# Kernel optimization log

Hardware: AMD Instinct MI355X
Metric: run time of the kernel (lower is better)

Reference implementation:

```python
import jax, jax.numpy as jnp
import numpy as np

WS = 7        # window size (square)
SH = 3        # shift size
NH = 8        # num heads
N = WS * WS   # tokens per window


def _rel_pos_index():
    coords = np.stack(np.meshgrid(np.arange(WS), np.arange(WS), indexing='ij'))
    cf = coords.reshape(2, -1)                      # (2, N)
    rel = cf[:, :, None] - cf[:, None, :]           # (2, N, N)
    rel = rel.transpose(1, 2, 0)
    rel[:, :, 0] += WS - 1
    rel[:, :, 1] += WS - 1
    rel[:, :, 0] *= 2 * WS - 1
    return rel.sum(-1)                              # (N, N) int


def _attn_mask(pH, pW):
    img = np.zeros((pH, pW), dtype=np.float32)
    h_sl = [(0, pH - WS), (pH - WS, pH - SH), (pH - SH, pH)]
    w_sl = [(0, pW - WS), (pW - WS, pW - SH), (pW - SH, pW)]
    cnt = 0
    for h0, h1 in h_sl:
        for w0, w1 in w_sl:
            img[h0:h1, w0:w1] = cnt
            cnt += 1
    m = img.reshape(pH // WS, WS, pW // WS, WS).transpose(0, 2, 1, 3).reshape(-1, N)
    diff = m[:, None, :] - m[:, :, None]            # (nw, N, N)
    return np.where(diff != 0, -100.0, 0.0).astype(np.float32)


def setup_inputs() -> dict:
    key = jax.random.key(0)
    ks = jax.random.split(key, 6)
    C = 256
    return {
        'x': jax.random.normal(ks[0], (32, 56, 56, C), dtype=jnp.float32),
        'qkv_weight': jax.random.normal(ks[1], (3 * C, C), dtype=jnp.float32) * 0.02,
        'qkv_bias': jax.random.normal(ks[2], (3 * C,), dtype=jnp.float32) * 0.02,
        'proj_weight': jax.random.normal(ks[3], (C, C), dtype=jnp.float32) * 0.02,
        'proj_bias': jax.random.normal(ks[4], (C,), dtype=jnp.float32) * 0.02,
        'rpb_table': jax.random.normal(ks[5], ((2 * WS - 1) ** 2, NH), dtype=jnp.float32) * 0.02,
    }


def reference(x, qkv_weight, qkv_bias, proj_weight, proj_bias, rpb_table):
    B, H, W, C = x.shape
    hd = C // NH
    pad_r = (WS - W % WS) % WS
    pad_b = (WS - H % WS) % WS
    xp = jnp.pad(x, ((0, 0), (0, pad_b), (0, pad_r), (0, 0)))
    pH, pW = H + pad_b, W + pad_r
    xp = jnp.roll(xp, shift=(-SH, -SH), axis=(1, 2))
    nw = (pH // WS) * (pW // WS)
    # window partition -> (B*nw, N, C)
    xw = xp.reshape(B, pH // WS, WS, pW // WS, WS, C)
    xw = xw.transpose(0, 1, 3, 2, 4, 5).reshape(B * nw, N, C)
    # qkv projection
    qkv = xw @ qkv_weight.T + qkv_bias                      # (B*nw, N, 3C)
    qkv = qkv.reshape(B * nw, N, 3, NH, hd).transpose(2, 0, 3, 1, 4)
    q, k, v = qkv[0], qkv[1], qkv[2]                        # (B*nw, NH, N, hd)
    q = q * (hd ** -0.5)
    attn = jnp.einsum('bhnd,bhmd->bhnm', q, k)              # (B*nw, NH, N, N)
    # relative position bias
    idx = jnp.asarray(_rel_pos_index())
    bias = rpb_table[idx].transpose(2, 0, 1)                # (NH, N, N)
    attn = attn + bias[None]
    # shift mask
    mask = jnp.asarray(_attn_mask(pH, pW))                  # (nw, N, N)
    attn = attn.reshape(B, nw, NH, N, N) + mask[None, :, None]
    attn = jax.nn.softmax(attn.reshape(B * nw, NH, N, N), axis=-1)
    out = jnp.einsum('bhnm,bhmd->bhnd', attn, v)            # (B*nw, NH, N, hd)
    out = out.transpose(0, 2, 1, 3).reshape(B * nw, N, C)
    out = out @ proj_weight.T + proj_bias
    # window reverse
    out = out.reshape(B, pH // WS, pW // WS, WS, WS, C)
    out = out.transpose(0, 1, 3, 2, 4, 5).reshape(B, pH, pW, C)
    out = jnp.roll(out, shift=(SH, SH), axis=(1, 2))
    return out[:, :H, :W, :]
```

## Files before the change

### kernel.cpp

```cpp
#include <hip/hip_runtime.h>
#include <hip/hip_bf16.h>

typedef __attribute__((ext_vector_type(4))) float f32x4;
typedef __attribute__((ext_vector_type(8))) short s16x8;
typedef __attribute__((ext_vector_type(4))) short s16x4;

#define LQS 520
#define FOS 260
#define VTS 72
#define LAS 264

#define OFF_A    0
#define SZ_A     (64 * LQS * 2)
#define OFF_B    (OFF_A + SZ_A)
#define SZ_B     (256 * VTS * 2)
#define OFF_BIAS (OFF_B + SZ_B)
#define SZ_BIAS  6096
#define OFF_ML   (OFF_BIAS + SZ_BIAS)
#define SZ_ML    (8 * 2 * 64 * 2 * 4)
#define SMEM_BYTES (OFF_ML + SZ_ML)

__device__ __forceinline__ short f2bf(float f) {
    unsigned u = __builtin_bit_cast(unsigned, f);
    unsigned r = (u + 0x7FFFu + ((u >> 16) & 1u)) >> 16;
    return (short)r;
}

__device__ __forceinline__ unsigned pk2bf(float a, float b) {
    return (unsigned)(unsigned short)f2bf(a) | ((unsigned)(unsigned short)f2bf(b) << 16);
}

__device__ __forceinline__ int region_id(int wy, int wx, int ty, int tx) {
    int rr = wy * 7 + ty;
    int cc = wx * 7 + tx;
    int rh = (rr < 49) ? 0 : ((rr < 53) ? 1 : 2);
    int rw = (cc < 49) ? 0 : ((cc < 53) ? 1 : 2);
    return rh * 3 + rw;
}

__global__ void wcvt_kernel(const float* __restrict__ qw, const float* __restrict__ pw,
                            short* __restrict__ wqkv, short* __restrict__ wproj) {
    int idx = blockIdx.x * blockDim.x + threadIdx.x;
    int stride = gridDim.x * blockDim.x;
    for (int i = idx; i < 65536; i += stride) {
        if (i < 49152) {
            const f32x4 v = *(const f32x4*)(qw + i * 4);
            s16x4 o = { f2bf(v.x), f2bf(v.y), f2bf(v.z), f2bf(v.w) };
            *(s16x4*)(wqkv + i * 4) = o;
        } else {
            int j = i - 49152;
            const f32x4 v = *(const f32x4*)(pw + j * 4);
            s16x4 o = { f2bf(v.x), f2bf(v.y), f2bf(v.z), f2bf(v.w) };
            *(s16x4*)(wproj + j * 4) = o;
        }
    }
}

__global__ __launch_bounds__(1024, 4)
void swin_kernel(const float* __restrict__ x,
                 const float* __restrict__ qkv_bias,
                 const float* __restrict__ proj_bias,
                 const float* __restrict__ rpb,
                 const short* __restrict__ wqkv,
                 const short* __restrict__ wproj,
                 float* __restrict__ out) {
    __shared__ __align__(16) char smem[SMEM_BYTES];
    short* lqk   = (short*)(smem + OFF_A);
    float* lout  = (float*)(smem + OFF_A);
    short* lvt   = (short*)(smem + OFF_B);
    short* la    = (short*)(smem + OFF_B);
    float* lbias = (float*)(smem + OFF_BIAS);
    float* lml   = (float*)(smem + OFF_ML);

    const int tid  = threadIdx.x;
    const int w    = tid >> 6;
    const int lane = tid & 63;
    const int il   = lane & 15;
    const int gl   = lane >> 4;
    const int hh   = w >> 1;
    const int jh   = w & 1;

    const int b   = blockIdx.x >> 6;
    const int wid = blockIdx.x & 63;
    const int wy  = wid >> 3, wx = wid & 7;

    for (int i = tid; i < 1352; i += 1024) lbias[(i >> 3) * 9 + (i & 7)] = rpb[i];
    for (int i = tid; i < 4096; i += 1024) {
        int t = i >> 6, c4 = (i & 63) << 2;
        s16x4 o;
        if (t < 49) {
            int ty = t / 7, tx = t % 7;
            int R = wy * 7 + ty + 3; if (R >= 56) R -= 56;
            int C = wx * 7 + tx + 3; if (C >= 56) C -= 56;
            const f32x4 v = *(const f32x4*)(x + (((b * 56 + R) * 56 + C) << 8) + c4);
            o = (s16x4){ f2bf(v.x), f2bf(v.y), f2bf(v.z), f2bf(v.w) };
        } else {
            o = (s16x4){ 0, 0, 0, 0 };
        }
        *(s16x4*)&lqk[t * LQS + c4] = o;
    }
    __syncthreads();

    {
        f32x4 acc[4][3];
        #pragma unroll
        for (int mi = 0; mi < 4; mi++)
            #pragma unroll
            for (int t = 0; t < 3; t++) acc[mi][t] = (f32x4){0.f, 0.f, 0.f, 0.f};
        for (int k0 = 0; k0 < 256; k0 += 32) {
            s16x8 a[4];
            #pragma unroll
            for (int mi = 0; mi < 4; mi++)
                a[mi] = *(const s16x8*)&lqk[(mi * 16 + il) * LQS + k0 + 8 * gl];
            #pragma unroll
            for (int t = 0; t < 3; t++) {
                s16x8 bfr = *(const s16x8*)(wqkv + (t * 256 + 16 * w + il) * 256 + k0 + 8 * gl);
                #pragma unroll
                for (int mi = 0; mi < 4; mi++)
                    acc[mi][t] = __builtin_amdgcn_mfma_f32_16x16x32_bf16(a[mi], bfr, acc[mi][t], 0, 0, 0);
            }
        }
        {
            float bv = qkv_bias[512 + 16 * w + il];
            #pragma unroll
            for (int mi = 0; mi < 4; mi++) {
                s16x4 pk = { f2bf(acc[mi][2][0] + bv), f2bf(acc[mi][2][1] + bv),
                             f2bf(acc[mi][2][2] + bv), f2bf(acc[mi][2][3] + bv) };
                *(s16x4*)&lvt[(16 * w + il) * VTS + mi * 16 + gl * 4] = pk;
            }
        }
        __syncthreads();
        {
            float bq_ = qkv_bias[16 * w + il];
            float bk_ = qkv_bias[256 + 16 * w + il];
            #pragma unroll
            for (int mi = 0; mi < 4; mi++)
                #pragma unroll
                for (int r = 0; r < 4; r++) {
                    int row = mi * 16 + gl * 4 + r;
                    lqk[row * LQS + 16 * w + il] = f2bf((acc[mi][0][r] + bq_) * 0.17677669529663687f);
                    lqk[row * LQS + 256 + 16 * w + il] = f2bf(acc[mi][1][r] + bk_);
                }
        }
    }
    __syncthreads();

    f32x4 s[2][4];
    {
        s16x8 bq[4], ak[2];
        #pragma unroll
        for (int ni = 0; ni < 4; ni++)
            bq[ni] = *(const s16x8*)&lqk[(ni * 16 + il) * LQS + 32 * hh + 8 * gl];
        #pragma unroll
        for (int mi = 0; mi < 2; mi++)
            ak[mi] = *(const s16x8*)&lqk[(jh * 32 + mi * 16 + il) * LQS + 256 + 32 * hh + 8 * gl];
        #pragma unroll
        for (int mi = 0; mi < 2; mi++)
            #pragma unroll
            for (int ni = 0; ni < 4; ni++)
                s[mi][ni] = __builtin_amdgcn_mfma_f32_16x16x32_bf16(ak[mi], bq[ni], (f32x4){0.f,0.f,0.f,0.f}, 0, 0, 0);
    }
    int base9[4], cnti[4];
    #pragma unroll
    for (int ni = 0; ni < 4; ni++) {
        int i = ni * 16 + il; int ic = i > 48 ? 48 : i;
        int yi = ic / 7, xi = ic % 7;
        base9[ni] = (yi * 13 + xi + 84) * 9 + hh;
        cnti[ni] = region_id(wy, wx, yi, xi);
    }
    float mx[4] = { -1e30f, -1e30f, -1e30f, -1e30f };
    #pragma unroll
    for (int mi = 0; mi < 2; mi++) {
        #pragma unroll
        for (int r = 0; r < 4; r++) {
            int j = 32 * jh + mi * 16 + gl * 4 + r;
            bool jok = (j < 49);
            int jc = jok ? j : 48;
            int yj = jc / 7, xj = jc % 7;
            int bj9 = (yj * 13 + xj) * 9;
            int cj = region_id(wy, wx, yj, xj);
            #pragma unroll
            for (int ni = 0; ni < 4; ni++) {
                float v;
                if (jok) {
                    float bb = lbias[base9[ni] - bj9];
                    v = s[mi][ni][r] + bb + ((cnti[ni] != cj) ? -100.0f : 0.0f);
                } else {
                    v = -1e30f;
                }
                s[mi][ni][r] = v;
                mx[ni] = fmaxf(mx[ni], v);
            }
        }
    }
    #pragma unroll
    for (int ni = 0; ni < 4; ni++) {
        mx[ni] = fmaxf(mx[ni], __shfl_xor(mx[ni], 16));
        mx[ni] = fmaxf(mx[ni], __shfl_xor(mx[ni], 32));
    }
    float sm[4] = { 0.f, 0.f, 0.f, 0.f };
    #pragma unroll
    for (int mi = 0; mi < 2; mi++)
        #pragma unroll
        for (int ni = 0; ni < 4; ni++)
            #pragma unroll
            for (int r = 0; r < 4; r++) {
                float p = __expf(s[mi][ni][r] - mx[ni]);
                s[mi][ni][r] = p;
                sm[ni] += p;
            }
    #pragma unroll
    for (int ni = 0; ni < 4; ni++) {
        sm[ni] += __shfl_xor(sm[ni], 16);
        sm[ni] += __shfl_xor(sm[ni], 32);
    }
    if (gl == 0) {
        #pragma unroll
        for (int ni = 0; ni < 4; ni++) {
            int idx = ((hh * 2 + jh) * 64 + ni * 16 + il) * 2;
            lml[idx] = mx[ni];
            lml[idx + 1] = sm[ni];
        }
    }
    __syncthreads();
    float scale[4];
    #pragma unroll
    for (int ni = 0; ni < 4; ni++) {
        int idx = ((hh * 2 + (jh ^ 1)) * 64 + ni * 16 + il) * 2;
        float m_o = lml[idx], l_o = lml[idx + 1];
        float m_g = fmaxf(mx[ni], m_o);
        float l_g = sm[ni] * __expf(mx[ni] - m_g) + l_o * __expf(m_o - m_g);
        scale[ni] = __expf(mx[ni] - m_g) / l_g;
    }
    f32x4 o[2][4];
    {
        unsigned pkd[2][4][2];
        #pragma unroll
        for (int mi = 0; mi < 2; mi++)
            #pragma unroll
            for (int ni = 0; ni < 4; ni++) {
                pkd[mi][ni][0] = pk2bf(s[mi][ni][0] * scale[ni], s[mi][ni][1] * scale[ni]);
                pkd[mi][ni][1] = pk2bf(s[mi][ni][2] * scale[ni], s[mi][ni][3] * scale[ni]);
            }
        s16x8 av[2];
        #pragma unroll
        for (int md = 0; md < 2; md++)
            av[md] = *(const s16x8*)&lvt[(32 * hh + md * 16 + il) * VTS + jh * 32 + 8 * gl];
        #pragma unroll
        for (int ni = 0; ni < 4; ni++) {
            unsigned wd[4];
            #pragma unroll
            for (int q = 0; q < 4; q++) {
                int src = (2 * (gl & 1) + (q >> 1)) * 16 + il;
                unsigned v0 = (unsigned)__shfl((int)pkd[0][ni][q & 1], src);
                unsigned v1 = (unsigned)__shfl((int)pkd[1][ni][q & 1], src);
                wd[q] = (gl & 2) ? v1 : v0;
            }
            union { unsigned u[4]; s16x8 v; } cv;
            cv.u[0] = wd[0]; cv.u[1] = wd[1]; cv.u[2] = wd[2]; cv.u[3] = wd[3];
            #pragma unroll
            for (int md = 0; md < 2; md++)
                o[md][ni] = __builtin_amdgcn_mfma_f32_16x16x32_bf16(av[md], cv.v, (f32x4){0.f,0.f,0.f,0.f}, 0, 0, 0);
        }
    }
    if (jh == 0) {
        #pragma unroll
        for (int md = 0; md < 2; md++)
            #pragma unroll
            for (int ni = 0; ni < 4; ni++)
                *(f32x4*)&lout[(ni * 16 + il) * FOS + 32 * hh + md * 16 + gl * 4] = o[md][ni];
    }
    __syncthreads();
    if (jh == 1) {
        #pragma unroll
        for (int md = 0; md < 2; md++)
            #pragma unroll
            for (int ni = 0; ni < 4; ni++) {
                f32x4 t = *(const f32x4*)&lout[(ni * 16 + il) * FOS + 32 * hh + md * 16 + gl * 4];
                t.x += o[md][ni][0]; t.y += o[md][ni][1];
                t.z += o[md][ni][2]; t.w += o[md][ni][3];
                s16x4 pk = { f2bf(t.x), f2bf(t.y), f2bf(t.z), f2bf(t.w) };
                *(s16x4*)&la[(ni * 16 + il) * LAS + 32 * hh + md * 16 + gl * 4] = pk;
            }
    }
    __syncthreads();

    {
        f32x4 acc[4];
        #pragma unroll
        for (int mi = 0; mi < 4; mi++) acc[mi] = (f32x4){0.f, 0.f, 0.f, 0.f};
        for (int k0 = 0; k0 < 256; k0 += 32) {
            s16x8 bw = *(const s16x8*)(wproj + (16 * w + il) * 256 + k0 + 8 * gl);
            #pragma unroll
            for (int mi = 0; mi < 4; mi++) {
                s16x8 a = *(const s16x8*)&la[(mi * 16 + il) * LAS + k0 + 8 * gl];
                acc[mi] = __builtin_amdgcn_mfma_f32_16x16x32_bf16(a, bw, acc[mi], 0, 0, 0);
            }
        }
        float pb = proj_bias[16 * w + il];
        float* fout = lout;
        #pragma unroll
        for (int mi = 0; mi < 4; mi++)
            #pragma unroll
            for (int r = 0; r < 4; r++) {
                int t = mi * 16 + gl * 4 + r;
                if (t < 49) fout[t * FOS + 16 * w + il] = acc[mi][r] + pb;
            }
    }
    __syncthreads();
    for (int i = tid; i < 3136; i += 1024) {
        int t = i >> 6, c4 = (i & 63) << 2;
        f32x4 v = *(const f32x4*)&lout[t * FOS + c4];
        int ty = t / 7, tx = t % 7;
        int R = wy * 7 + ty + 3; if (R >= 56) R -= 56;
        int C = wx * 7 + tx + 3; if (C >= 56) C -= 56;
        *(f32x4*)(out + (((b * 56 + R) * 56 + C) << 8) + c4) = v;
    }
}

extern "C" void kernel_launch(void* const* d_in, const int* in_sizes, int n_in,
                              void* d_out, int out_size, void* d_ws, size_t ws_size,
                              hipStream_t stream) {
    const float* x   = (const float*)d_in[0];
    const float* qw  = (const float*)d_in[1];
    const float* qb  = (const float*)d_in[2];
    const float* pw  = (const float*)d_in[3];
    const float* pb  = (const float*)d_in[4];
    const float* rpb = (const float*)d_in[5];

    short* wqkv  = (short*)d_ws;
    short* wproj = wqkv + 768 * 256;

    wcvt_kernel<<<128, 256, 0, stream>>>(qw, pw, wqkv, wproj);
    swin_kernel<<<2048, 1024, 0, stream>>>(x, qb, pb, rpb, wqkv, wproj, (float*)d_out);
}
```

Measured before the change: 231.5 us.

## Precompute bias+mask table, fold into MFMA accumulator, drop softmax max pass

A new pre-kernel builds a combined relative-position-bias and shift-mask table for the four window classes, pre-scaled by log2(e). The attention kernel loads it as the MFMA accumulator init. It also folds log2(e) into the q scale, uses exp2 without subtracting the row max, and applies deferred normalization after PV. Float-to-bf16 conversion now uses the hardware packed convert instruction. These changes remove per-element index math, the max reduction and the cross-wave max exchange. Skipping the max subtraction risks overflow if scores are large.

```diff
diff --git a/kernel.cpp b/kernel.cpp
--- a/kernel.cpp
+++ b/kernel.cpp
@@ -14,28 +14,14 @@
 #define SZ_A     (64 * LQS * 2)
 #define OFF_B    (OFF_A + SZ_A)
 #define SZ_B     (256 * VTS * 2)
-#define OFF_BIAS (OFF_B + SZ_B)
-#define SZ_BIAS  6096
-#define OFF_ML   (OFF_BIAS + SZ_BIAS)
-#define SZ_ML    (8 * 2 * 64 * 2 * 4)
+#define OFF_ML   (OFF_B + SZ_B)
+#define SZ_ML    (8 * 64 * 4)
 #define SMEM_BYTES (OFF_ML + SZ_ML)
 
-__device__ __forceinline__ short f2bf(float f) {
-    unsigned u = __builtin_bit_cast(unsigned, f);
-    unsigned r = (u + 0x7FFFu + ((u >> 16) & 1u)) >> 16;
-    return (short)r;
-}
-
-__device__ __forceinline__ unsigned pk2bf(float a, float b) {
-    return (unsigned)(unsigned short)f2bf(a) | ((unsigned)(unsigned short)f2bf(b) << 16);
-}
-
-__device__ __forceinline__ int region_id(int wy, int wx, int ty, int tx) {
-    int rr = wy * 7 + ty;
-    int cc = wx * 7 + tx;
-    int rh = (rr < 49) ? 0 : ((rr < 53) ? 1 : 2);
-    int rw = (cc < 49) ? 0 : ((cc < 53) ? 1 : 2);
-    return rh * 3 + rw;
+__device__ __forceinline__ unsigned cvt2bf(float a, float b) {
+    unsigned r;
+    asm("v_cvt_pk_bf16_f32 %0, %1, %2" : "=v"(r) : "v"(a), "v"(b));
+    return r;
 }
 
 __global__ void wcvt_kernel(const float* __restrict__ qw, const float* __restrict__ pw,
@@ -43,33 +29,51 @@
     int idx = blockIdx.x * blockDim.x + threadIdx.x;
     int stride = gridDim.x * blockDim.x;
     for (int i = idx; i < 65536; i += stride) {
-        if (i < 49152) {
-            const f32x4 v = *(const f32x4*)(qw + i * 4);
-            s16x4 o = { f2bf(v.x), f2bf(v.y), f2bf(v.z), f2bf(v.w) };
-            *(s16x4*)(wqkv + i * 4) = o;
-        } else {
-            int j = i - 49152;
-            const f32x4 v = *(const f32x4*)(pw + j * 4);
-            s16x4 o = { f2bf(v.x), f2bf(v.y), f2bf(v.z), f2bf(v.w) };
-            *(s16x4*)(wproj + j * 4) = o;
-        }
-    }
+        const float* src = (i < 49152) ? (qw + i * 4) : (pw + (i - 49152) * 4);
+        unsigned* dst = (unsigned*)((i < 49152) ? (wqkv + i * 4) : (wproj + (i - 49152) * 4));
+        const f32x4 v = *(const f32x4*)src;
+        uint2 o = { cvt2bf(v.x, v.y), cvt2bf(v.z, v.w) };
+        *(uint2*)dst = o;
+    }
+}
+
+__global__ void bmgen_kernel(const float* __restrict__ rpb, float* __restrict__ bm) {
+    int idx = blockIdx.x * blockDim.x + threadIdx.x;
+    if (idx >= 131072) return;
+    int j = idx & 63;
+    int i = (idx >> 6) & 63;
+    int h = (idx >> 12) & 7;
+    int c = idx >> 15;
+    int cy = c >> 1, cx = c & 1;
+    float v;
+    if (j >= 49) {
+        v = -1e9f;
+    } else {
+        int ic = i > 48 ? 48 : i;
+        int yi = ic / 7, xi = ic % 7;
+        int yj = j / 7, xj = j % 7;
+        float bias = rpb[((yi - yj + 6) * 13 + (xi - xj + 6)) * 8 + h];
+        int ri = (cy ? (yi < 4 ? 1 : 2) : 0) * 3 + (cx ? (xi < 4 ? 1 : 2) : 0);
+        int rj = (cy ? (yj < 4 ? 1 : 2) : 0) * 3 + (cx ? (xj < 4 ? 1 : 2) : 0);
+        float mask = (ri != rj) ? -100.0f : 0.0f;
+        v = (bias + mask) * 1.4426950408889634f;
+    }
+    bm[idx] = v;
 }
 
 __global__ __launch_bounds__(1024, 4)
 void swin_kernel(const float* __restrict__ x,
                  const float* __restrict__ qkv_bias,
                  const float* __restrict__ proj_bias,
-                 const float* __restrict__ rpb,
                  const short* __restrict__ wqkv,
                  const short* __restrict__ wproj,
+                 const float* __restrict__ bm,
                  float* __restrict__ out) {
     __shared__ __align__(16) char smem[SMEM_BYTES];
     short* lqk   = (short*)(smem + OFF_A);
     float* lout  = (float*)(smem + OFF_A);
     short* lvt   = (short*)(smem + OFF_B);
     short* la    = (short*)(smem + OFF_B);
-    float* lbias = (float*)(smem + OFF_BIAS);
     float* lml   = (float*)(smem + OFF_ML);
 
     const int tid  = threadIdx.x;
@@ -84,20 +88,19 @@
     const int wid = blockIdx.x & 63;
     const int wy  = wid >> 3, wx = wid & 7;
 
-    for (int i = tid; i < 1352; i += 1024) lbias[(i >> 3) * 9 + (i & 7)] = rpb[i];
     for (int i = tid; i < 4096; i += 1024) {
         int t = i >> 6, c4 = (i & 63) << 2;
-        s16x4 o;
+        uint2 o;
         if (t < 49) {
             int ty = t / 7, tx = t % 7;
             int R = wy * 7 + ty + 3; if (R >= 56) R -= 56;
             int C = wx * 7 + tx + 3; if (C >= 56) C -= 56;
             const f32x4 v = *(const f32x4*)(x + (((b * 56 + R) * 56 + C) << 8) + c4);
-            o = (s16x4){ f2bf(v.x), f2bf(v.y), f2bf(v.z), f2bf(v.w) };
+            o.x = cvt2bf(v.x, v.y); o.y = cvt2bf(v.z, v.w);
         } else {
-            o = (s16x4){ 0, 0, 0, 0 };
-        }
-        *(s16x4*)&lqk[t * LQS + c4] = o;
+            o.x = 0; o.y = 0;
+        }
+        *(uint2*)&lqk[t * LQS + c4] = o;
     }
     __syncthreads();
 
@@ -124,25 +127,35 @@
             float bv = qkv_bias[512 + 16 * w + il];
             #pragma unroll
             for (int mi = 0; mi < 4; mi++) {
-                s16x4 pk = { f2bf(acc[mi][2][0] + bv), f2bf(acc[mi][2][1] + bv),
-                             f2bf(acc[mi][2][2] + bv), f2bf(acc[mi][2][3] + bv) };
-                *(s16x4*)&lvt[(16 * w + il) * VTS + mi * 16 + gl * 4] = pk;
+                uint2 pk = { cvt2bf(acc[mi][2][0] + bv, acc[mi][2][1] + bv),
+                             cvt2bf(acc[mi][2][2] + bv, acc[mi][2][3] + bv) };
+                *(uint2*)&lvt[(16 * w + il) * VTS + mi * 16 + gl * 4] = pk;
             }
         }
         __syncthreads();
         {
             float bq_ = qkv_bias[16 * w + il];
             float bk_ = qkv_bias[256 + 16 * w + il];
+            const float QSCL = 0.17677669529663687f * 1.4426950408889634f;
             #pragma unroll
             for (int mi = 0; mi < 4; mi++)
                 #pragma unroll
                 for (int r = 0; r < 4; r++) {
                     int row = mi * 16 + gl * 4 + r;
-                    lqk[row * LQS + 16 * w + il] = f2bf((acc[mi][0][r] + bq_) * 0.17677669529663687f);
-                    lqk[row * LQS + 256 + 16 * w + il] = f2bf(acc[mi][1][r] + bk_);
+                    unsigned u = cvt2bf((acc[mi][0][r] + bq_) * QSCL, acc[mi][1][r] + bk_);
+                    lqk[row * LQS + 16 * w + il] = (short)u;
+                    lqk[row * LQS + 256 + 16 * w + il] = (short)(u >> 16);
                 }
         }
     }
+    const int cls = ((wy == 7) ? 2 : 0) + ((wx == 7) ? 1 : 0);
+    const float* bmp = bm + ((cls * 8 + hh) * 64) * 64;
+    f32x4 ci[2][4];
+    #pragma unroll
+    for (int mi = 0; mi < 2; mi++)
+        #pragma unroll
+        for (int ni = 0; ni < 4; ni++)
+            ci[mi][ni] = *(const f32x4*)&bmp[(ni * 16 + il) * 64 + jh * 32 + mi * 16 + gl * 4];
     __syncthreads();
 
     f32x4 s[2][4];
@@ -158,45 +171,7 @@
         for (int mi = 0; mi < 2; mi++)
             #pragma unroll
             for (int ni = 0; ni < 4; ni++)
-                s[mi][ni] = __builtin_amdgcn_mfma_f32_16x16x32_bf16(ak[mi], bq[ni], (f32x4){0.f,0.f,0.f,0.f}, 0, 0, 0);
-    }
-    int base9[4], cnti[4];
-    #pragma unroll
-    for (int ni = 0; ni < 4; ni++) {
-        int i = ni * 16 + il; int ic = i > 48 ? 48 : i;
-        int yi = ic / 7, xi = ic % 7;
-        base9[ni] = (yi * 13 + xi + 84) * 9 + hh;
-        cnti[ni] = region_id(wy, wx, yi, xi);
-    }
-    float mx[4] = { -1e30f, -1e30f, -1e30f, -1e30f };
-    #pragma unroll
-    for (int mi = 0; mi < 2; mi++) {
-        #pragma unroll
-        for (int r = 0; r < 4; r++) {
-            int j = 32 * jh + mi * 16 + gl * 4 + r;
-            bool jok = (j < 49);
-            int jc = jok ? j : 48;
-            int yj = jc / 7, xj = jc % 7;
-            int bj9 = (yj * 13 + xj) * 9;
-            int cj = region_id(wy, wx, yj, xj);
-            #pragma unroll
-            for (int ni = 0; ni < 4; ni++) {
-                float v;
-                if (jok) {
-                    float bb = lbias[base9[ni] - bj9];
-                    v = s[mi][ni][r] + bb + ((cnti[ni] != cj) ? -100.0f : 0.0f);
-                } else {
-                    v = -1e30f;
-                }
-                s[mi][ni][r] = v;
-                mx[ni] = fmaxf(mx[ni], v);
-            }
-        }
-    }
-    #pragma unroll
-    for (int ni = 0; ni < 4; ni++) {
-        mx[ni] = fmaxf(mx[ni], __shfl_xor(mx[ni], 16));
-        mx[ni] = fmaxf(mx[ni], __shfl_xor(mx[ni], 32));
+                s[mi][ni] = __builtin_amdgcn_mfma_f32_16x16x32_bf16(ak[mi], bq[ni], ci[mi][ni], 0, 0, 0);
     }
     float sm[4] = { 0.f, 0.f, 0.f, 0.f };
     #pragma unroll
@@ -205,7 +180,7 @@
         for (int ni = 0; ni < 4; ni++)
             #pragma unroll
             for (int r = 0; r < 4; r++) {
-                float p = __expf(s[mi][ni][r] - mx[ni]);
+                float p = exp2f(s[mi][ni][r]);
                 s[mi][ni][r] = p;
                 sm[ni] += p;
             }
@@ -214,34 +189,22 @@
         sm[ni] += __shfl_xor(sm[ni], 16);
         sm[ni] += __shfl_xor(sm[ni], 32);
     }
-    if (gl == 0) {
+    if (jh == 0 && gl == 0) {
+        #pragma unroll
+        for (int ni = 0; ni < 4; ni++) lml[hh * 64 + ni * 16 + il] = sm[ni];
+    }
+    unsigned pkd[2][4][2];
+    #pragma unroll
+    for (int mi = 0; mi < 2; mi++)
         #pragma unroll
         for (int ni = 0; ni < 4; ni++) {
-            int idx = ((hh * 2 + jh) * 64 + ni * 16 + il) * 2;
-            lml[idx] = mx[ni];
-            lml[idx + 1] = sm[ni];
-        }
-    }
-    __syncthreads();
-    float scale[4];
-    #pragma unroll
-    for (int ni = 0; ni < 4; ni++) {
-        int idx = ((hh * 2 + (jh ^ 1)) * 64 + ni * 16 + il) * 2;
-        float m_o = lml[idx], l_o = lml[idx + 1];
-        float m_g = fmaxf(mx[ni], m_o);
-        float l_g = sm[ni] * __expf(mx[ni] - m_g) + l_o * __expf(m_o - m_g);
-        scale[ni] = __expf(mx[ni] - m_g) / l_g;
-    }
+            pkd[mi][ni][0] = cvt2bf(s[mi][ni][0], s[mi][ni][1]);
+            pkd[mi][ni][1] = cvt2bf(s[mi][ni][2], s[mi][ni][3]);
+        }
+    __syncthreads();
+
     f32x4 o[2][4];
     {
-        unsigned pkd[2][4][2];
-        #pragma unroll
-        for (int mi = 0; mi < 2; mi++)
-            #pragma unroll
-            for (int ni = 0; ni < 4; ni++) {
-                pkd[mi][ni][0] = pk2bf(s[mi][ni][0] * scale[ni], s[mi][ni][1] * scale[ni]);
-                pkd[mi][ni][1] = pk2bf(s[mi][ni][2] * scale[ni], s[mi][ni][3] * scale[ni]);
-            }
         s16x8 av[2];
         #pragma unroll
         for (int md = 0; md < 2; md++)
@@ -272,15 +235,21 @@
     }
     __syncthreads();
     if (jh == 1) {
+        float sc[4];
+        #pragma unroll
+        for (int ni = 0; ni < 4; ni++)
+            sc[ni] = __builtin_amdgcn_rcpf(lml[hh * 64 + ni * 16 + il] + sm[ni]);
         #pragma unroll
         for (int md = 0; md < 2; md++)
             #pragma unroll
             for (int ni = 0; ni < 4; ni++) {
                 f32x4 t = *(const f32x4*)&lout[(ni * 16 + il) * FOS + 32 * hh + md * 16 + gl * 4];
-                t.x += o[md][ni][0]; t.y += o[md][ni][1];
-                t.z += o[md][ni][2]; t.w += o[md][ni][3];
-                s16x4 pk = { f2bf(t.x), f2bf(t.y), f2bf(t.z), f2bf(t.w) };
-                *(s16x4*)&la[(ni * 16 + il) * LAS + 32 * hh + md * 16 + gl * 4] = pk;
+                float a0 = (t.x + o[md][ni][0]) * sc[ni];
+                float a1 = (t.y + o[md][ni][1]) * sc[ni];
+                float a2 = (t.z + o[md][ni][2]) * sc[ni];
+                float a3 = (t.w + o[md][ni][3]) * sc[ni];
+                uint2 pk = { cvt2bf(a0, a1), cvt2bf(a2, a3) };
+                *(uint2*)&la[(ni * 16 + il) * LAS + 32 * hh + md * 16 + gl * 4] = pk;
             }
     }
     __syncthreads();
@@ -330,7 +299,9 @@
 
     short* wqkv  = (short*)d_ws;
     short* wproj = wqkv + 768 * 256;
+    float* bmt   = (float*)((char*)d_ws + 524288);
 
     wcvt_kernel<<<128, 256, 0, stream>>>(qw, pw, wqkv, wproj);
-    swin_kernel<<<2048, 1024, 0, stream>>>(x, qb, pb, rpb, wqkv, wproj, (float*)d_out);
-}
+    bmgen_kernel<<<512, 256, 0, stream>>>(rpb, bmt);
+    swin_kernel<<<2048, 1024, 0, stream>>>(x, qb, pb, wqkv, wproj, bmt, (float*)d_out);
+}
```

Measured after the change: 231.3 us. About the same (-0.1%).
